# Performance work log

Hardware: AMD Instinct MI355X
Metric: run time of the kernel (lower is better)

The kernel has to match this reference:

```python
import jax, jax.numpy as jnp
import numpy as np
from jax import lax

B, FREQ, T = 4, 258, 2176
N_FRAMES, N_SHIFT = 128, 64
W = 32            # number of spectral windows: 128 + 64*k < 2176
H = 5 * 28 * 14   # 1960
NUM_CLASSES = 2


def setup_inputs() -> dict:
    key = jax.random.key(0)
    ks = jax.random.split(key, 13)
    x = jax.random.normal(ks[0], (B, FREQ, T), jnp.float32)
    hx0 = jax.random.normal(ks[1], (B, H), jnp.float32)
    labels = jax.random.randint(ks[2], (B,), 0, NUM_CLASSES, jnp.int64)
    conv1_w = jax.random.normal(ks[3], (64, 1, 9, 9), jnp.float32) * 0.05
    conv1_b = jax.random.normal(ks[4], (64,), jnp.float32) * 0.05
    conv2_w = jax.random.normal(ks[5], (5, 64, 4, 4), jnp.float32) * 0.05
    conv2_b = jax.random.normal(ks[6], (5,), jnp.float32) * 0.05
    w_ih = jax.random.normal(ks[7], (3 * H, H), jnp.float32) * 0.02
    w_hh = jax.random.normal(ks[8], (3 * H, H), jnp.float32) * 0.02
    b_ih = jax.random.normal(ks[9], (3 * H,), jnp.float32) * 0.02
    b_hh = jax.random.normal(ks[10], (3 * H,), jnp.float32) * 0.02
    fc_w = jax.random.normal(ks[11], (NUM_CLASSES, H), jnp.float32) * 0.02
    fc_b = jax.random.normal(ks[12], (NUM_CLASSES,), jnp.float32) * 0.02
    return dict(x=x, hx0=hx0, labels=labels, conv1_w=conv1_w, conv1_b=conv1_b,
                conv2_w=conv2_w, conv2_b=conv2_b, w_ih=w_ih, w_hh=w_hh,
                b_ih=b_ih, b_hh=b_hh, fc_w=fc_w, fc_b=fc_b)


def _conv_sig_pool(y, w, b, pad):
    y = lax.conv_general_dilated(y, w, (1, 1), [(pad, pad), (pad, pad)],
                                 dimension_numbers=('NCHW', 'OIHW', 'NCHW'))
    y = jax.nn.sigmoid(y + b[None, :, None, None])
    return lax.reduce_window(y, -jnp.inf, lax.max, (1, 1, 3, 3), (1, 1, 3, 3), 'VALID')


def reference(x, hx0, labels, conv1_w, conv1_b, conv2_w, conv2_b,
              w_ih, w_hh, b_ih, b_hh, fc_w, fc_b):
    # spectral windows: drop first freq bin, slide window of 128 frames, stride 64
    loc = x[:, 1:, :]                                   # [B, 257, T]
    idx = jnp.arange(W)[:, None] * N_SHIFT + jnp.arange(N_FRAMES)[None, :]
    win = loc[:, :, idx]                                # [B, 257, W, 128]
    win = win.transpose(0, 2, 1, 3).reshape(B * W, 1, 257, N_FRAMES)

    y = _conv_sig_pool(win, conv1_w, conv1_b, 2)        # [B*W, 64, 84, 41]
    y = _conv_sig_pool(y, conv2_w, conv2_b, 2)          # [B*W, 5, 28, 14]
    feat = y.reshape(B, W, H)                           # flatten C,H,W (C-order)

    def gru_step(h, xt):                                # xt: [B, H]
        gi = xt @ w_ih.T + b_ih                         # [B, 3H]
        gh = h @ w_hh.T + b_hh
        i_r, i_z, i_n = jnp.split(gi, 3, axis=1)
        h_r, h_z, h_n = jnp.split(gh, 3, axis=1)
        r = jax.nn.sigmoid(i_r + h_r)
        z = jax.nn.sigmoid(i_z + h_z)
        n = jnp.tanh(i_n + r * h_n)
        return (1.0 - z) * n + z * h, None

    hT, _ = lax.scan(gru_step, hx0, feat.transpose(1, 0, 2))  # scan over W steps

    logits = hT @ fc_w.T + fc_b                         # [B, num_classes]
    samples = jax.nn.softmax(logits, axis=1)
    return (samples, labels)
```

## Files before the change

### kernel.cpp

```cpp
#include <hip/hip_runtime.h>
#include <hip/hip_cooperative_groups.h>

__device__ __forceinline__ float bf2f(unsigned short u) {
  union { unsigned int i; float f; } v; v.i = ((unsigned int)u) << 16; return v.f;
}
__device__ __forceinline__ unsigned short f2bf(float f) {
  union { float f; unsigned int i; } v; v.f = f;
  unsigned int x = v.i;
  return (unsigned short)((x + 0x7fffu + ((x >> 16) & 1u)) >> 16);
}
__device__ __forceinline__ float sigmf(float x) { return 1.f / (1.f + __expf(-x)); }
__device__ __forceinline__ float tanhfast(float x) {
  float xc = fminf(fmaxf(x, -15.f), 15.f);
  float e = __expf(2.f * xc);
  return (e - 1.f) / (e + 1.f);
}

typedef float f32x4 __attribute__((ext_vector_type(4)));
typedef short short8v __attribute__((ext_vector_type(8)));
typedef short short4v __attribute__((ext_vector_type(4)));

__device__ __forceinline__ short8v pack8(const float* p) {
  union { short8v s; unsigned int u[4]; } r;
#pragma unroll
  for (int i = 0; i < 4; ++i) {
    unsigned int lo = __float_as_uint(p[2 * i]) >> 16;
    unsigned int hi = __float_as_uint(p[2 * i + 1]) & 0xFFFF0000u;
    r.u[i] = hi | lo;
  }
  return r.s;
}

#define KP 1984
#define NP 5888
#define GRU_BLOCKS 245
#define C1_PLANE 2860

__global__ void k_prep(const float* __restrict__ w1, const float* __restrict__ b1,
                       unsigned short* __restrict__ w1f,
                       const float* __restrict__ w2, unsigned short* __restrict__ w2f,
                       unsigned short* __restrict__ feat_bf,
                       unsigned long long* __restrict__ hb0,
                       unsigned long long* __restrict__ hb1) {
  const int b = blockIdx.x;
  const int tid = threadIdx.x;
  if (b < 24) {
    int idx = b * 256 + tid;
    if (idx < 4 * 3 * 64 * 8) {
      int j = idx & 7, l = (idx >> 3) & 63;
      int rest = idx >> 9;
      int s = rest % 3, ocf = rest / 3;
      int oc = ocf * 16 + (l & 15);
      int k = s * 32 + (l >> 4) * 8 + j;
      float v = 0.f;
      if (k < 64)       v = w1[oc * 81 + (k >> 3) * 9 + (k & 7)];
      else if (k < 72)  v = w1[oc * 81 + 72 + (k - 64)];
      else if (k < 80)  v = w1[oc * 81 + (k - 72) * 9 + 8];
      else if (k == 80) v = w1[oc * 81 + 80];
      else if (k == 81) v = b1[oc];
      w1f[idx] = f2bf(v);
    }
  } else if (b < 88) {
    int idx = (b - 24) * 256 + tid;
    if (idx < 32 * 64 * 8) {
      int j = idx & 7, l = (idx >> 3) & 63, s = idx >> 9;
      int oc = l & 15;
      int k = s * 32 + (l >> 4) * 8 + j;
      int t = k >> 6, ch = k & 63, fr = t >> 2, fc = t & 3;
      float v = (oc < 5) ? w2[((oc * 64 + ch) * 4 + fr) * 4 + fc] : 0.f;
      w2f[idx] = f2bf(v);
    }
  } else {
    for (int i = tid; i < 128 * 24; i += 256) {
      int n = i / 24, k = 1960 + i % 24;
      feat_bf[(size_t)n * KP + k] = 0;
    }
    for (int i = tid; i < 3920; i += 256) {
      hb0[i] = 0ull;
      hb1[i] = 0ull;
    }
  }
}

__global__ __launch_bounds__(256) void k_conv1(const float* __restrict__ x,
                                               const unsigned short* __restrict__ w1f,
                                               unsigned short* __restrict__ pool1) {
  const int n = blockIdx.x, qrg = blockIdx.y;
  const int b = n >> 5, w = n & 31;
  __shared__ __align__(16) unsigned short s_b[4 * C1_PLANE];
  const int tid = threadIdx.x;
  for (int i = tid; i < 20 * 132; i += 256) {
    int lr = i / 132, lc = i % 132;
    int f = 12 * qrg + lr - 2;
    int t = lc - 2;
    float v = 0.f;
    if (f >= 0 && f < 257 && t >= 0 && t < 128)
      v = x[((size_t)b * 258 + 1 + f) * 2176 + w * 64 + t];
    unsigned short bf = f2bf(v);
#pragma unroll
    for (int m = 0; m < 4; ++m) s_b[m * C1_PLANE + lr * 140 + lc + m] = bf;
  }
  const int lane = tid & 63, wv = tid >> 6;
  short8v bw[4][3];
#pragma unroll
  for (int ocf = 0; ocf < 4; ++ocf)
#pragma unroll
    for (int s = 0; s < 3; ++s)
      bw[ocf][s] = *reinterpret_cast<const short8v*>(&w1f[(((ocf * 3) + s) * 64 + lane) * 8]);
  __syncthreads();

  const int qr = qrg * 4 + wv;
  const int li = lane & 15, g = lane >> 4;

  for (int pgt = 0; pgt < 3; ++pgt) {
    int pg = pgt * 16 + li;
    if (pg > 40) pg = 40;
    f32x4 pm[4];
#pragma unroll
    for (int ocf = 0; ocf < 4; ++ocf) pm[ocf] = (f32x4){-3.4e38f, -3.4e38f, -3.4e38f, -3.4e38f};

    for (int rr = 0; rr < 3; ++rr) {
      const int lrb = 3 * wv + rr;
#pragma unroll
      for (int phi = 0; phi < 3; ++phi) {
        const int c = 3 * pg + phi;
        const int m = (-c) & 3;
        const unsigned short* hb = &s_b[m * C1_PLANE + c + m];
        f32x4 acc[4];
#pragma unroll
        for (int ocf = 0; ocf < 4; ++ocf) acc[ocf] = (f32x4){0.f, 0.f, 0.f, 0.f};
        const unsigned short* p0 = hb + (lrb + g) * 140;
        short8v a0 = __builtin_shufflevector(*reinterpret_cast<const short4v*>(p0),
                                             *reinterpret_cast<const short4v*>(p0 + 4),
                                             0, 1, 2, 3, 4, 5, 6, 7);
#pragma unroll
        for (int ocf = 0; ocf < 4; ++ocf)
          acc[ocf] = __builtin_amdgcn_mfma_f32_16x16x32_bf16(a0, bw[ocf][0], acc[ocf], 0, 0, 0);
        const unsigned short* p1 = p0 + 4 * 140;
        short8v a1 = __builtin_shufflevector(*reinterpret_cast<const short4v*>(p1),
                                             *reinterpret_cast<const short4v*>(p1 + 4),
                                             0, 1, 2, 3, 4, 5, 6, 7);
#pragma unroll
        for (int ocf = 0; ocf < 4; ++ocf)
          acc[ocf] = __builtin_amdgcn_mfma_f32_16x16x32_bf16(a1, bw[ocf][1], acc[ocf], 0, 0, 0);
        short8v a2;
        if (g == 0) {
          const unsigned short* p2 = p0 + 8 * 140;
          a2 = __builtin_shufflevector(*reinterpret_cast<const short4v*>(p2),
                                       *reinterpret_cast<const short4v*>(p2 + 4),
                                       0, 1, 2, 3, 4, 5, 6, 7);
        } else if (g == 1) {
          const unsigned short* pv = &s_b[lrb * 140 + c + 8];
          union { short8v s8; unsigned int u[4]; } r;
          r.u[0] = (unsigned)pv[0]       | ((unsigned)pv[140] << 16);
          r.u[1] = (unsigned)pv[2 * 140] | ((unsigned)pv[3 * 140] << 16);
          r.u[2] = (unsigned)pv[4 * 140] | ((unsigned)pv[5 * 140] << 16);
          r.u[3] = (unsigned)pv[6 * 140] | ((unsigned)pv[7 * 140] << 16);
          a2 = r.s8;
        } else if (g == 2) {
          union { short8v s8; unsigned int u[4]; } r;
          r.u[0] = (unsigned)s_b[(lrb + 8) * 140 + c + 8] | 0x3F800000u;
          r.u[1] = 0; r.u[2] = 0; r.u[3] = 0;
          a2 = r.s8;
        } else {
          a2 = (short8v){0, 0, 0, 0, 0, 0, 0, 0};
        }
#pragma unroll
        for (int ocf = 0; ocf < 4; ++ocf)
          acc[ocf] = __builtin_amdgcn_mfma_f32_16x16x32_bf16(a2, bw[ocf][2], acc[ocf], 0, 0, 0);
#pragma unroll
        for (int ocf = 0; ocf < 4; ++ocf) {
#pragma unroll
          for (int i = 0; i < 4; ++i) pm[ocf][i] = fmaxf(pm[ocf][i], acc[ocf][i]);
        }
      }
    }
#pragma unroll
    for (int ocf = 0; ocf < 4; ++ocf) {
#pragma unroll
      for (int i = 0; i < 4; ++i) {
        int pg2 = pgt * 16 + g * 4 + i;
        if (pg2 <= 40) {
          int oc = ocf * 16 + li;
          pool1[(((size_t)n * 84 + qr) * 41 + pg2) * 64 + oc] = f2bf(sigmf(pm[ocf][i]));
        }
      }
    }
  }
}

__global__ __launch_bounds__(128, 2) void k_conv2(const unsigned short* __restrict__ pool1,
                                                  const unsigned short* __restrict__ w2f,
                                                  const float* __restrict__ b2,
                                                  unsigned short* __restrict__ feat_bf) {
  const int n = blockIdx.x, qg = blockIdx.y;
  __shared__ __align__(16) unsigned short s_a[9 * 46 * 64];
  const int tid = threadIdx.x;
  const int lane = tid & 63, wv = tid >> 6;
  short8v bwr[32];
#pragma unroll
  for (int s = 0; s < 32; ++s)
    bwr[s] = *reinterpret_cast<const short8v*>(&w2f[(s * 64 + lane) * 8]);
  const int r0 = 6 * qg - 2;
  for (int idx = tid; idx < 9 * 46 * 8; idx += 128) {
    int row = idx / (46 * 8);
    int rem = idx - row * (46 * 8);
    int lc = rem >> 3, cp = rem & 7;
    int gr = r0 + row, gc = lc - 2;
    short8v v = {0, 0, 0, 0, 0, 0, 0, 0};
    if ((unsigned)gr < 84u && (unsigned)gc < 41u)
      v = *reinterpret_cast<const short8v*>(&pool1[(((size_t)n * 84 + gr) * 41 + gc) * 64 + cp * 8]);
    int rot = (cp * 8 + lc * 8) & 63;
    *reinterpret_cast<short8v*>(&s_a[(row * 46 + lc) * 64 + rot]) = v;
  }
  __syncthreads();

  const int q = qg * 2 + wv;
  const int li = lane & 15, g = lane >> 4;
  const int pg = li > 13 ? 13 : li;
  f32x4 pm = (f32x4){-3.4e38f, -3.4e38f, -3.4e38f, -3.4e38f};

  for (int rr = 0; rr < 3; ++rr) {
#pragma unroll
    for (int phi = 0; phi < 3; ++phi) {
      f32x4 acc[4];
#pragma unroll
      for (int i = 0; i < 4; ++i) acc[i] = (f32x4){0.f, 0.f, 0.f, 0.f};
#pragma unroll
      for (int s = 0; s < 32; ++s) {
        const int t = s >> 1, h = s & 1;
        const int fr = t >> 2, fc = t & 3;
        const int srow = 3 * wv + rr + fr;
        const int lc = 3 * pg + phi + fc;
        const int rot = (h * 32 + g * 8 + lc * 8) & 63;
        short8v a = *reinterpret_cast<const short8v*>(&s_a[(srow * 46 + lc) * 64 + rot]);
        acc[s & 3] = __builtin_amdgcn_mfma_f32_16x16x32_bf16(a, bwr[s], acc[s & 3], 0, 0, 0);
      }
      f32x4 sum;
#pragma unroll
      for (int i = 0; i < 4; ++i) sum[i] = (acc[0][i] + acc[1][i]) + (acc[2][i] + acc[3][i]);
#pragma unroll
      for (int i = 0; i < 4; ++i) pm[i] = fmaxf(pm[i], sum[i]);
    }
  }
  if (li < 5) {
#pragma unroll
    for (int i = 0; i < 4; ++i) {
      int pq = g * 4 + i;
      if (pq < 14)
        feat_bf[(size_t)n * KP + li * 392 + q * 14 + pq] = f2bf(sigmf(pm[i] + b2[li]));
    }
  }
}

__global__ __launch_bounds__(256) void k_gi(const unsigned short* __restrict__ feat_bf,
                                            const float* __restrict__ w_ih,
                                            const float* __restrict__ b_ih,
                                            float* __restrict__ gi) {
  const int bx = blockIdx.x, bm = blockIdx.y;
  const int w = threadIdx.x >> 6, lane = threadIdx.x & 63;
  const int li = lane & 15, g = lane >> 4;
  const int j = bx * 16 + li;
  const int jc = j < 5880 ? j : 5879;
  const unsigned short* ap = feat_bf + (size_t)(bm * 64 + w * 16 + li) * KP + g * 8;
  const float* bp = w_ih + (size_t)jc * 1960 + g * 8;
  const short8v z8 = {0, 0, 0, 0, 0, 0, 0, 0};
  f32x4 acc0 = (f32x4){0.f, 0.f, 0.f, 0.f};
  f32x4 acc1 = (f32x4){0.f, 0.f, 0.f, 0.f};
  for (int kc = 0; kc < 62; kc += 2) {
    short8v a0 = *reinterpret_cast<const short8v*>(ap + kc * 32);
    short8v a1 = *reinterpret_cast<const short8v*>(ap + kc * 32 + 32);
    short8v b0 = pack8(bp + kc * 32);
    short8v b1 = (kc != 60 || g == 0) ? pack8(bp + kc * 32 + 32) : z8;
    acc0 = __builtin_amdgcn_mfma_f32_16x16x32_bf16(a0, b0, acc0, 0, 0, 0);
    acc1 = __builtin_amdgcn_mfma_f32_16x16x32_bf16(a1, b1, acc1, 0, 0, 0);
  }
  if (j < 5880) {
    const float bi = b_ih[j];
    const int n0 = bm * 64 + w * 16 + g * 4;
#pragma unroll
    for (int i = 0; i < 4; ++i)
      gi[(size_t)(n0 + i) * 5880 + j] = acc0[i] + acc1[i] + bi;
  }
}

__global__ __launch_bounds__(512) void k_gru(const float* __restrict__ whh,
                                             const float* __restrict__ b_hh,
                                             const float* __restrict__ gi,
                                             const float* __restrict__ hx0,
                                             unsigned long long* __restrict__ hb0,
                                             unsigned long long* __restrict__ hb1,
                                             const float* __restrict__ fc_w,
                                             const float* __restrict__ fc_b,
                                             const int* __restrict__ labels,
                                             float* __restrict__ out) {
  __shared__ __align__(16) unsigned short s_w[2 * 62 * 64 * 8];
  __shared__ __align__(16) unsigned short s_h[4 * 1984];
  __shared__ float s_part[4 * 2 * 64 * 4];
  __shared__ float s_gi[96];
  const int tid = threadIdx.x;
  const int bid = blockIdx.x;
  const int k0 = bid * 8;
  const int lane = tid & 63, wv = tid >> 6;
  const int li = lane & 15, g2 = lane >> 4;

  for (int idx = tid; idx < 2 * 62 * 64; idx += 512) {
    int mt = idx / 3968;
    int rem = idx - mt * 3968;
    int kc = rem >> 6, l = rem & 63;
    int lli = l & 15, lg2 = l >> 4;
    int k = kc * 32 + lg2 * 8;
    short8v v = {0, 0, 0, 0, 0, 0, 0, 0};
    bool rowok = (mt == 0) ? true : (lli < 8);
    if (rowok && k < 1960) {
      int g = (mt == 0) ? (lli >> 3) : 2;
      int kk = (mt == 0) ? (lli & 7) : lli;
      v = pack8(&whh[(size_t)(g * 1960 + k0 + kk) * 1960 + k]);
    }
    *reinterpret_cast<short8v*>(&s_w[(size_t)idx * 8]) = v;
  }
  for (int i = tid; i < 4 * 992; i += 512) reinterpret_cast<unsigned int*>(s_h)[i] = 0u;

  float hp0 = 0.f, hp1 = 0.f, bhr0 = 0, bhr1 = 0, bhz0 = 0, bhz1 = 0, bhn0 = 0, bhn1 = 0;
  if (tid < 16) {
    int cb = tid >> 2, p = tid & 3;
    int k = k0 + 2 * p;
    hp0 = hx0[cb * 1960 + k];
    hp1 = hx0[cb * 1960 + k + 1];
    bhr0 = b_hh[k];         bhr1 = b_hh[k + 1];
    bhz0 = b_hh[1960 + k];  bhz1 = b_hh[1960 + k + 1];
    bhn0 = b_hh[3920 + k];  bhn1 = b_hh[3920 + k + 1];
  }
  __syncthreads();

  for (int t = 0; t < 32; ++t) {
    if (t == 0) {
      for (int i = tid; i < 7840; i += 512) {
        int b = i / 1960, k = i - b * 1960;
        s_h[b * 1984 + k] = f2bf(hx0[i]);
      }
    } else {
      const unsigned long long* hin = (t & 1) ? hb1 : hb0;
      unsigned pend = 0;
#pragma unroll
      for (int r = 0; r < 8; ++r)
        if (tid + (r << 9) < 3920) pend |= (1u << r);
      while (pend) {
        unsigned long long v[8];
#pragma unroll
        for (int r = 0; r < 8; ++r)
          if (pend & (1u << r))
            v[r] = __hip_atomic_load(&hin[tid + (r << 9)], __ATOMIC_RELAXED,
                                     __HIP_MEMORY_SCOPE_AGENT);
#pragma unroll
        for (int r = 0; r < 8; ++r) {
          if ((pend & (1u << r)) && (unsigned)(v[r] >> 32) >= (unsigned)t) {
            int i = tid + (r << 9);
            int b = i / 980, kp = i - b * 980;
            reinterpret_cast<unsigned int*>(s_h)[b * 992 + kp] = (unsigned)v[r];
            pend &= ~(1u << r);
          }
        }
        if (pend) __builtin_amdgcn_s_sleep(0);
      }
    }
    if (tid < 96) {
      int gg = tid >> 5, bb = (tid >> 3) & 3, kk = tid & 7;
      s_gi[tid] = gi[(size_t)(bb * 32 + t) * 5880 + gg * 1960 + k0 + kk];
    }
    __syncthreads();

    if (wv < 4) {
      f32x4 acc0 = (f32x4){0.f, 0.f, 0.f, 0.f};
      f32x4 acc1 = (f32x4){0.f, 0.f, 0.f, 0.f};
      for (int kc = wv; kc < 62; kc += 4) {
        short8v bfr = *reinterpret_cast<const short8v*>(&s_h[(li & 3) * 1984 + kc * 32 + g2 * 8]);
        short8v a0 = *reinterpret_cast<const short8v*>(&s_w[((size_t)kc * 64 + lane) * 8]);
        short8v a1 = *reinterpret_cast<const short8v*>(&s_w[((size_t)(62 + kc) * 64 + lane) * 8]);
        acc0 = __builtin_amdgcn_mfma_f32_16x16x32_bf16(a0, bfr, acc0, 0, 0, 0);
        acc1 = __builtin_amdgcn_mfma_f32_16x16x32_bf16(a1, bfr, acc1, 0, 0, 0);
      }
      *reinterpret_cast<f32x4*>(&s_part[((wv * 2 + 0) * 64 + lane) * 4]) = acc0;
      *reinterpret_cast<f32x4*>(&s_part[((wv * 2 + 1) * 64 + lane) * 4]) = acc1;
    }
    __syncthreads();

    unsigned long long* hout = (t & 1) ? hb0 : hb1;
    if (tid < 16) {
      const int cb = tid >> 2, p = tid & 3;
      const int kk = 2 * p;
      auto psum = [&](int mt, int m) -> float {
        int base = mt * 256 + ((m >> 2) * 16 + cb) * 4 + (m & 3);
        return ((s_part[base] + s_part[base + 512]) +
                (s_part[base + 1024] + s_part[base + 1536]));
      };
      float ghr0 = psum(0, kk),     ghr1 = psum(0, kk + 1);
      float ghz0 = psum(0, 8 + kk), ghz1 = psum(0, 8 + kk + 1);
      float ghn0 = psum(1, kk),     ghn1 = psum(1, kk + 1);
      float r0 = sigmf(s_gi[cb * 8 + kk] + ghr0 + bhr0);
      float z0 = sigmf(s_gi[32 + cb * 8 + kk] + ghz0 + bhz0);
      float n0 = tanhfast(s_gi[64 + cb * 8 + kk] + r0 * (ghn0 + bhn0));
      float h0v = (1.f - z0) * n0 + z0 * hp0;
      float r1 = sigmf(s_gi[cb * 8 + kk + 1] + ghr1 + bhr1);
      float z1 = sigmf(s_gi[32 + cb * 8 + kk + 1] + ghz1 + bhz1);
      float n1 = tanhfast(s_gi[64 + cb * 8 + kk + 1] + r1 * (ghn1 + bhn1));
      float h1v = (1.f - z1) * n1 + z1 * hp1;
      hp0 = h0v; hp1 = h1v;
      unsigned long long packed =
          ((unsigned long long)(unsigned)(t + 1) << 32) |
          (unsigned long long)((unsigned)f2bf(h0v) | ((unsigned)f2bf(h1v) << 16));
      __hip_atomic_store(&hout[cb * 980 + (k0 >> 1) + p], packed,
                         __ATOMIC_RELAXED, __HIP_MEMORY_SCOPE_AGENT);
    }
    __syncthreads();
  }

  if (bid == 0) {
    unsigned pend = 0;
#pragma unroll
    for (int r = 0; r < 8; ++r)
      if (tid + (r << 9) < 3920) pend |= (1u << r);
    while (pend) {
      unsigned long long v[8];
#pragma unroll
      for (int r = 0; r < 8; ++r)
        if (pend & (1u << r))
          v[r] = __hip_atomic_load(&hb0[tid + (r << 9)], __ATOMIC_RELAXED,
                                   __HIP_MEMORY_SCOPE_AGENT);
#pragma unroll
      for (int r = 0; r < 8; ++r) {
        if ((pend & (1u << r)) && (unsigned)(v[r] >> 32) >= 32u) {
          int i = tid + (r << 9);
          int b = i / 980, kp = i - b * 980;
          reinterpret_cast<unsigned int*>(s_h)[b * 992 + kp] = (unsigned)v[r];
          pend &= ~(1u << r);
        }
      }
      if (pend) __builtin_amdgcn_s_sleep(0);
    }
    __syncthreads();
    if (tid < 64) {
      const int l = tid;
      float acc[8];
#pragma unroll
      for (int i = 0; i < 8; ++i) acc[i] = 0.f;
      for (int k = l; k < 1960; k += 64) {
        const float w0 = fc_w[k], w1 = fc_w[1960 + k];
#pragma unroll
        for (int b = 0; b < 4; ++b) {
          const float hv = bf2f(s_h[b * 1984 + k]);
          acc[b * 2 + 0] += hv * w0;
          acc[b * 2 + 1] += hv * w1;
        }
      }
#pragma unroll
      for (int i = 0; i < 8; ++i) {
        float a = acc[i];
#pragma unroll
        for (int off = 32; off; off >>= 1) a += __shfl_xor(a, off, 64);
        acc[i] = a;
      }
      if (l == 0) {
#pragma unroll
        for (int b = 0; b < 4; ++b) {
          const float l0 = acc[b * 2] + fc_b[0], l1 = acc[b * 2 + 1] + fc_b[1];
          const float m = fmaxf(l0, l1);
          const float e0 = __expf(l0 - m), e1 = __expf(l1 - m);
          const float s = e0 + e1;
          out[b * 2 + 0] = e0 / s;
          out[b * 2 + 1] = e1 / s;
        }
        for (int i = 0; i < 4; ++i) out[8 + i] = (float)labels[i];
      }
    }
  }
}

extern "C" void kernel_launch(void* const* d_in, const int* in_sizes, int n_in,
                              void* d_out, int out_size, void* d_ws, size_t ws_size,
                              hipStream_t stream) {
  const float* x       = (const float*)d_in[0];
  const float* hx0     = (const float*)d_in[1];
  const int*   labels  = (const int*)d_in[2];
  const float* conv1_w = (const float*)d_in[3];
  const float* conv1_b = (const float*)d_in[4];
  const float* conv2_w = (const float*)d_in[5];
  const float* conv2_b = (const float*)d_in[6];
  const float* w_ih    = (const float*)d_in[7];
  const float* w_hh    = (const float*)d_in[8];
  const float* b_ih    = (const float*)d_in[9];
  const float* b_hh    = (const float*)d_in[10];
  const float* fc_w    = (const float*)d_in[11];
  const float* fc_b    = (const float*)d_in[12];

  char* ws = (char*)d_ws;
  size_t off = 0;
  unsigned short* pool1 = (unsigned short*)(ws + off); off += (size_t)128 * 84 * 41 * 64 * 2;
  unsigned short* feat_bf = (unsigned short*)(ws + off); off += (size_t)128 * KP * 2;
  float* gi    = (float*)(ws + off); off += (size_t)128 * 5880 * 4;
  unsigned long long* hb0 = (unsigned long long*)(ws + off); off += (size_t)4 * 980 * 8;
  unsigned long long* hb1 = (unsigned long long*)(ws + off); off += (size_t)4 * 980 * 8;
  unsigned short* w1f = (unsigned short*)(ws + off); off += (size_t)4 * 3 * 64 * 8 * 2;
  unsigned short* w2f = (unsigned short*)(ws + off); off += (size_t)32 * 64 * 8 * 2;

  k_prep<<<89, 256, 0, stream>>>(conv1_w, conv1_b, w1f, conv2_w, w2f, feat_bf, hb0, hb1);

  dim3 g1(128, 21);
  k_conv1<<<g1, 256, 0, stream>>>(x, w1f, pool1);

  dim3 g2(128, 14);
  k_conv2<<<g2, 128, 0, stream>>>(pool1, w2f, conv2_b, feat_bf);

  dim3 g3(368, 2);
  k_gi<<<g3, 256, 0, stream>>>(feat_bf, w_ih, b_ih, gi);

  void* gru_args[] = {(void*)&w_hh, (void*)&b_hh, (void*)&gi, (void*)&hx0,
                      (void*)&hb0, (void*)&hb1, (void*)&fc_w, (void*)&fc_b,
                      (void*)&labels, (void*)&d_out};
  hipLaunchCooperativeKernel((const void*)k_gru, dim3(GRU_BLOCKS), dim3(512), gru_args, 0, stream);
}
```

Measured before the change: 372.4 us.

## Pre-convert W_hh to bf16 in prep kernel and drop per-step GRU barrier

Adds a bulk fp32-to-bf16 conversion of the recurrent weight matrix to the prep kernel, so the cooperative GRU kernel loads pre-packed bf16 vectors into LDS instead of reading fp32 and packing. The intent is to move the weight-staging cost off the serial GRU critical path into a highly parallel kernel. It also double-buffers the per-step input-gate shared buffer so the trailing __syncthreads at the end of each timestep can be removed. The costs are an extra full pass over W_hh (read fp32, write bf16) and reliance on the next iteration's barrier ordering to keep shared buffers safe. The conversion also changes truncation to round-to-nearest.

```diff
diff --git a/kernel.cpp b/kernel.cpp
--- a/kernel.cpp
+++ b/kernel.cpp
@@ -32,11 +32,11 @@
 }
 
 #define KP 1984
-#define NP 5888
 #define GRU_BLOCKS 245
 #define C1_PLANE 2860
 
-__global__ void k_prep(const float* __restrict__ w1, const float* __restrict__ b1,
+__global__ void k_prep(const float* __restrict__ w_hh, unsigned short* __restrict__ whh_bf,
+                       const float* __restrict__ w1, const float* __restrict__ b1,
                        unsigned short* __restrict__ w1f,
                        const float* __restrict__ w2, unsigned short* __restrict__ w2f,
                        unsigned short* __restrict__ feat_bf,
@@ -44,8 +44,16 @@
                        unsigned long long* __restrict__ hb1) {
   const int b = blockIdx.x;
   const int tid = threadIdx.x;
-  if (b < 24) {
-    int idx = b * 256 + tid;
+  if (b < 2048) {
+    const int n4 = 5880 * 1960 / 4;
+    for (int i = b * 256 + tid; i < n4; i += 2048 * 256) {
+      float4 v = *reinterpret_cast<const float4*>(&w_hh[i * 4]);
+      ushort4 u;
+      u.x = f2bf(v.x); u.y = f2bf(v.y); u.z = f2bf(v.z); u.w = f2bf(v.w);
+      *reinterpret_cast<ushort4*>(&whh_bf[i * 4]) = u;
+    }
+  } else if (b < 2072) {
+    int idx = (b - 2048) * 256 + tid;
     if (idx < 4 * 3 * 64 * 8) {
       int j = idx & 7, l = (idx >> 3) & 63;
       int rest = idx >> 9;
@@ -60,8 +68,8 @@
       else if (k == 81) v = b1[oc];
       w1f[idx] = f2bf(v);
     }
-  } else if (b < 88) {
-    int idx = (b - 24) * 256 + tid;
+  } else if (b < 2136) {
+    int idx = (b - 2072) * 256 + tid;
     if (idx < 32 * 64 * 8) {
       int j = idx & 7, l = (idx >> 3) & 63, s = idx >> 9;
       int oc = l & 15;
@@ -284,7 +292,7 @@
   }
 }
 
-__global__ __launch_bounds__(512) void k_gru(const float* __restrict__ whh,
+__global__ __launch_bounds__(512) void k_gru(const unsigned short* __restrict__ whh,
                                              const float* __restrict__ b_hh,
                                              const float* __restrict__ gi,
                                              const float* __restrict__ hx0,
@@ -297,7 +305,7 @@
   __shared__ __align__(16) unsigned short s_w[2 * 62 * 64 * 8];
   __shared__ __align__(16) unsigned short s_h[4 * 1984];
   __shared__ float s_part[4 * 2 * 64 * 4];
-  __shared__ float s_gi[96];
+  __shared__ float s_gi[2][96];
   const int tid = threadIdx.x;
   const int bid = blockIdx.x;
   const int k0 = bid * 8;
@@ -315,7 +323,7 @@
     if (rowok && k < 1960) {
       int g = (mt == 0) ? (lli >> 3) : 2;
       int kk = (mt == 0) ? (lli & 7) : lli;
-      v = pack8(&whh[(size_t)(g * 1960 + k0 + kk) * 1960 + k]);
+      v = *reinterpret_cast<const short8v*>(&whh[(size_t)(g * 1960 + k0 + kk) * 1960 + k]);
     }
     *reinterpret_cast<short8v*>(&s_w[(size_t)idx * 8]) = v;
   }
@@ -366,7 +374,7 @@
     }
     if (tid < 96) {
       int gg = tid >> 5, bb = (tid >> 3) & 3, kk = tid & 7;
-      s_gi[tid] = gi[(size_t)(bb * 32 + t) * 5880 + gg * 1960 + k0 + kk];
+      s_gi[t & 1][tid] = gi[(size_t)(bb * 32 + t) * 5880 + gg * 1960 + k0 + kk];
     }
     __syncthreads();
 
@@ -397,13 +405,13 @@
       float ghr0 = psum(0, kk),     ghr1 = psum(0, kk + 1);
       float ghz0 = psum(0, 8 + kk), ghz1 = psum(0, 8 + kk + 1);
       float ghn0 = psum(1, kk),     ghn1 = psum(1, kk + 1);
-      float r0 = sigmf(s_gi[cb * 8 + kk] + ghr0 + bhr0);
-      float z0 = sigmf(s_gi[32 + cb * 8 + kk] + ghz0 + bhz0);
-      float n0 = tanhfast(s_gi[64 + cb * 8 + kk] + r0 * (ghn0 + bhn0));
+      float r0 = sigmf(s_gi[t & 1][cb * 8 + kk] + ghr0 + bhr0);
+      float z0 = sigmf(s_gi[t & 1][32 + cb * 8 + kk] + ghz0 + bhz0);
+      float n0 = tanhfast(s_gi[t & 1][64 + cb * 8 + kk] + r0 * (ghn0 + bhn0));
       float h0v = (1.f - z0) * n0 + z0 * hp0;
-      float r1 = sigmf(s_gi[cb * 8 + kk + 1] + ghr1 + bhr1);
-      float z1 = sigmf(s_gi[32 + cb * 8 + kk + 1] + ghz1 + bhz1);
-      float n1 = tanhfast(s_gi[64 + cb * 8 + kk + 1] + r1 * (ghn1 + bhn1));
+      float r1 = sigmf(s_gi[t & 1][cb * 8 + kk + 1] + ghr1 + bhr1);
+      float z1 = sigmf(s_gi[t & 1][32 + cb * 8 + kk + 1] + ghz1 + bhz1);
+      float n1 = tanhfast(s_gi[t & 1][64 + cb * 8 + kk + 1] + r1 * (ghn1 + bhn1));
       float h1v = (1.f - z1) * n1 + z1 * hp1;
       hp0 = h0v; hp1 = h1v;
       unsigned long long packed =
@@ -412,7 +420,6 @@
       __hip_atomic_store(&hout[cb * 980 + (k0 >> 1) + p], packed,
                          __ATOMIC_RELAXED, __HIP_MEMORY_SCOPE_AGENT);
     }
-    __syncthreads();
   }
 
   if (bid == 0) {
@@ -498,12 +505,14 @@
   unsigned short* pool1 = (unsigned short*)(ws + off); off += (size_t)128 * 84 * 41 * 64 * 2;
   unsigned short* feat_bf = (unsigned short*)(ws + off); off += (size_t)128 * KP * 2;
   float* gi    = (float*)(ws + off); off += (size_t)128 * 5880 * 4;
+  unsigned short* whh_bf = (unsigned short*)(ws + off); off += (size_t)5880 * 1960 * 2;
   unsigned long long* hb0 = (unsigned long long*)(ws + off); off += (size_t)4 * 980 * 8;
   unsigned long long* hb1 = (unsigned long long*)(ws + off); off += (size_t)4 * 980 * 8;
   unsigned short* w1f = (unsigned short*)(ws + off); off += (size_t)4 * 3 * 64 * 8 * 2;
   unsigned short* w2f = (unsigned short*)(ws + off); off += (size_t)32 * 64 * 8 * 2;
 
-  k_prep<<<89, 256, 0, stream>>>(conv1_w, conv1_b, w1f, conv2_w, w2f, feat_bf, hb0, hb1);
+  k_prep<<<2137, 256, 0, stream>>>(w_hh, whh_bf, conv1_w, conv1_b, w1f,
+                                   conv2_w, w2f, feat_bf, hb0, hb1);
 
   dim3 g1(128, 21);
   k_conv1<<<g1, 256, 0, stream>>>(x, w1f, pool1);
@@ -514,7 +523,7 @@
   dim3 g3(368, 2);
   k_gi<<<g3, 256, 0, stream>>>(feat_bf, w_ih, b_ih, gi);
 
-  void* gru_args[] = {(void*)&w_hh, (void*)&b_hh, (void*)&gi, (void*)&hx0,
+  void* gru_args[] = {(void*)&whh_bf, (void*)&b_hh, (void*)&gi, (void*)&hx0,
                       (void*)&hb0, (void*)&hb1, (void*)&fc_w, (void*)&fc_b,
                       (void*)&labels, (void*)&d_out};
   hipLaunchCooperativeKernel((const void*)k_gru, dim3(GRU_BLOCKS), dim3(512), gru_args, 0, stream);
```

After: 418.8 us. 1.12x slower.
